# Optimization experiments

Measured on AMD Instinct MI355X. Metric: run time of the kernel, lower is better.

Reference implementation:

```python
import jax, jax.numpy as jnp
import numpy as np

FEAT = 36          # 4 + node_embedding_dim(32)
N_NODES = 24       # max_num_nodes_per_route
N_ROUTES = 48      # max_num_route
CUST_H = 128
CUST_OUT = 32
RNN_H = 128        # route_output_dim
B = 512


def _xavier(key, shape):
    fan_in, fan_out = shape[0], shape[1]
    lim = float(np.sqrt(6.0 / (fan_in + fan_out)))
    return jax.random.uniform(key, shape, jnp.float32, -lim, lim)


def setup_inputs() -> dict:
    key = jax.random.key(0)
    ks = jax.random.split(key, 24)
    inp = {
        "candidates": jax.random.normal(ks[0], (B, 2 * FEAT), jnp.float32),
        "customers": jax.random.normal(ks[1], (B, N_ROUTES, N_NODES * FEAT), jnp.float32),
        # Customer_Model MLP: 36 -> 128 (tanh) -> 32 (tanh)
        "cust_w1": _xavier(ks[2], (FEAT, CUST_H)),
        "cust_b1": jnp.zeros((CUST_H,), jnp.float32),
        "cust_w2": _xavier(ks[3], (CUST_H, CUST_OUT)),
        "cust_b2": jnp.zeros((CUST_OUT,), jnp.float32),
        # GRU layer 0 (input 32 -> hidden 128), gates order (r,z,n)
        "gru_wih0": _xavier(ks[4], (CUST_OUT, 3 * RNN_H)),
        "gru_whh0": _xavier(ks[5], (RNN_H, 3 * RNN_H)),
        "gru_bih0": jnp.zeros((3 * RNN_H,), jnp.float32),
        "gru_bhh0": jnp.zeros((3 * RNN_H,), jnp.float32),
        # GRU layer 1 (128 -> 128)
        "gru_wih1": _xavier(ks[6], (RNN_H, 3 * RNN_H)),
        "gru_whh1": _xavier(ks[7], (RNN_H, 3 * RNN_H)),
        "gru_bih1": jnp.zeros((3 * RNN_H,), jnp.float32),
        "gru_bhh1": jnp.zeros((3 * RNN_H,), jnp.float32),
        # candidate head and final MLP
        "cand_w": _xavier(ks[8], (2 * FEAT, 64)),
        "cand_b": jnp.zeros((64,), jnp.float32),
        "fc1_w": _xavier(ks[9], (RNN_H + 64, 128)),
        "fc1_b": jnp.zeros((128,), jnp.float32),
        "fc2_w": _xavier(ks[10], (128, 128)),
        "fc2_b": jnp.zeros((128,), jnp.float32),
        "fc3_w": _xavier(ks[11], (128, 1)),
        "fc3_b": jnp.zeros((1,), jnp.float32),
    }
    return inp


def _gru_layer(x_seq, wih, whh, bih, bhh):
    # x_seq: [T, N, in_dim]; returns [T, N, RNN_H]
    gi = jnp.einsum('tni,ih->tnh', x_seq, wih) + bih  # precompute input gates

    def step(h, gi_t):
        gh = h @ whh + bhh
        i_r, i_z, i_n = jnp.split(gi_t, 3, axis=-1)
        h_r, h_z, h_n = jnp.split(gh, 3, axis=-1)
        r = jax.nn.sigmoid(i_r + h_r)
        z = jax.nn.sigmoid(i_z + h_z)
        n = jnp.tanh(i_n + r * h_n)
        h_new = (1.0 - z) * n + z * h
        return h_new, h_new

    h0 = jnp.zeros((x_seq.shape[1], RNN_H), x_seq.dtype)
    _, out = jax.lax.scan(step, h0, gi)
    return out


def reference(candidates, customers, cust_w1, cust_b1, cust_w2, cust_b2,
              gru_wih0, gru_whh0, gru_bih0, gru_bhh0,
              gru_wih1, gru_whh1, gru_bih1, gru_bhh1,
              cand_w, cand_b, fc1_w, fc1_b, fc2_w, fc2_b, fc3_w, fc3_b):
    b = candidates.shape[0]
    x_c = candidates @ cand_w + cand_b                      # [B, 64]

    # all routes processed at once: fold routes into batch dim
    x = customers.reshape(b * N_ROUTES, N_NODES, FEAT)
    x = jnp.transpose(x, (1, 0, 2))                          # [T=24, B*48, 36]
    # Customer_Model MLP (tanh hidden, tanh output)
    x = jnp.tanh(jnp.tanh(x @ cust_w1 + cust_b1) @ cust_w2 + cust_b2)  # [24, B*48, 32]

    out = _gru_layer(x, gru_wih0, gru_whh0, gru_bih0, gru_bhh0)
    out = _gru_layer(out, gru_wih1, gru_whh1, gru_bih1, gru_bhh1)
    last = out[-1].reshape(b, N_ROUTES, RNN_H)               # last timestep per route
    x_r = last.mean(axis=1)                                  # mean over 48 routes
    # dropout is identity at inference

    h = jnp.concatenate([x_r, x_c], axis=1)                  # [B, 192]
    h = jnp.tanh(h @ fc1_w + fc1_b)
    h = jnp.tanh(h @ fc2_w + fc2_b)
    return h @ fc3_w + fc3_b                                 # [B, 1]
```

## Files before the change

### kernel.cpp

```cpp
#include <hip/hip_runtime.h>
#include <stdint.h>


#define NSEQ   24576
#define TSTEPS 24
#define SEQB   32

typedef __attribute__((ext_vector_type(8))) short bf16x8;
typedef __attribute__((ext_vector_type(4))) float floatx4;

#define PK_W1    0
#define PK_W2    8192
#define PK_WIH0  12288
#define PK_WHH0  24576
#define PK_WIH1  73728
#define PK_WHH1  122880
#define PK_END   172032
#define X2_EL    172032
#define HOUT_BYTE 38092800

#define MFMA(a,b,c) c = __builtin_amdgcn_mfma_f32_16x16x32_bf16(a, b, c, 0, 0, 0)

__device__ __forceinline__ uint16_t f2bf(float f) {
  uint32_t u = __float_as_uint(f);
  u += 0x7FFFu + ((u >> 16) & 1u);
  return (uint16_t)(u >> 16);
}
__device__ __forceinline__ uint32_t cvt_pk(float a, float b) {
  uint32_t r;
  asm("v_cvt_pk_bf16_f32 %0, %1, %2" : "=v"(r) : "v"(a), "v"(b));
  return r;
}
__device__ __forceinline__ float fast_sigmoid(float x) {
  float e = __builtin_amdgcn_exp2f(-1.4426950408889634f * x);
  return __builtin_amdgcn_rcpf(1.0f + e);
}
__device__ __forceinline__ float fast_tanh(float x) {
  float e = __builtin_amdgcn_exp2f(-2.8853900817779268f * x);
  return 2.0f * __builtin_amdgcn_rcpf(1.0f + e) - 1.0f;
}
__device__ __forceinline__ bf16x8 ldf(const uint16_t* p) {
  return *(const bf16x8*)p;
}

__global__ __launch_bounds__(256) void pack_weights(
    const float* __restrict__ w1, const float* __restrict__ w2,
    const float* __restrict__ wih0, const float* __restrict__ whh0,
    const float* __restrict__ wih1, const float* __restrict__ whh1,
    uint16_t* __restrict__ ws) {
  int idx = blockIdx.x * 256 + threadIdx.x;
  if (idx >= PK_END) return;
  const float* W; int N, KB, Kreal, base;
  if      (idx <  8192) { W = w1;   N = 128; KB = 2; Kreal = 36;  base = 0; }
  else if (idx < 12288) { W = w2;   N = 32;  KB = 4; Kreal = 128; base = 8192; }
  else if (idx < 24576) { W = wih0; N = 384; KB = 1; Kreal = 32;  base = 12288; }
  else if (idx < 73728) { W = whh0; N = 384; KB = 4; Kreal = 128; base = 24576; }
  else if (idx < 122880){ W = wih1; N = 384; KB = 4; Kreal = 128; base = 73728; }
  else                  { W = whh1; N = 384; KB = 4; Kreal = 128; base = 122880; }
  int li = idx - base;
  int frag = li >> 9;
  int e = li & 511;
  int lane = e >> 3, j = e & 7;
  int kb = frag % KB, nt = frag / KB;
  int k = kb * 32 + (lane >> 4) * 8 + j;
  int n = nt * 16 + (lane & 15);
  float v = (k < Kreal) ? W[k * N + n] : 0.0f;
  ws[base + li] = f2bf(v);
}

__global__ __launch_bounds__(256) void mlp_kernel(
    const float* __restrict__ customers, const float* __restrict__ b1,
    const float* __restrict__ b2, const uint16_t* __restrict__ wpk,
    uint16_t* __restrict__ x2out) {
  __shared__ uint16_t sA[128 * 136];
  const int r0 = blockIdx.x * 128;
  const int t  = r0 / NSEQ;
  const int s0 = r0 % NSEQ;
  const int tid = threadIdx.x;
  const int w = tid >> 6, l = tid & 63, q = l >> 4, c = l & 15;
  const int lo8 = l * 8;
  const int hb = 4 * q;

  floatx4 acc[2][8];
  #pragma unroll
  for (int mi = 0; mi < 2; ++mi)
    #pragma unroll
    for (int nt = 0; nt < 8; ++nt) acc[mi][nt] = (floatx4){0.f, 0.f, 0.f, 0.f};

  #pragma unroll
  for (int mi = 0; mi < 2; ++mi) {
    const int mt = 2 * w + mi;
    const int seq = s0 + mt * 16 + c;
    const float* xp = customers + (size_t)seq * 864 + t * 36;
    floatx4 u0 = *(const floatx4*)(xp + q * 8);
    floatx4 u1 = *(const floatx4*)(xp + q * 8 + 4);
    bf16x8 a0;
    { uint32_t* a0u = (uint32_t*)&a0;
      a0u[0] = cvt_pk(u0[0], u0[1]); a0u[1] = cvt_pk(u0[2], u0[3]);
      a0u[2] = cvt_pk(u1[0], u1[1]); a0u[3] = cvt_pk(u1[2], u1[3]); }
    bf16x8 a1x = (bf16x8){0,0,0,0,0,0,0,0};
    if (q == 0) {
      floatx4 u2 = *(const floatx4*)(xp + 32);
      uint32_t* a1u = (uint32_t*)&a1x;
      a1u[0] = cvt_pk(u2[0], u2[1]); a1u[1] = cvt_pk(u2[2], u2[3]);
    }
    #pragma unroll
    for (int nt = 0; nt < 8; ++nt) {
      bf16x8 bv0 = ldf(wpk + PK_W1 + (nt * 2 + 0) * 512 + lo8);
      bf16x8 bv1 = ldf(wpk + PK_W1 + (nt * 2 + 1) * 512 + lo8);
      MFMA(bv0, a0,  acc[mi][nt]);
      MFMA(bv1, a1x, acc[mi][nt]);
    }
  }
  #pragma unroll
  for (int mi = 0; mi < 2; ++mi) {
    const int mt = 2 * w + mi;
    #pragma unroll
    for (int nt = 0; nt < 8; ++nt) {
      const floatx4 bv = *(const floatx4*)(b1 + nt * 16 + hb);
      float o0 = fast_tanh(acc[mi][nt][0] + bv[0]);
      float o1 = fast_tanh(acc[mi][nt][1] + bv[1]);
      float o2 = fast_tanh(acc[mi][nt][2] + bv[2]);
      float o3 = fast_tanh(acc[mi][nt][3] + bv[3]);
      uint2 pk; pk.x = cvt_pk(o0, o1); pk.y = cvt_pk(o2, o3);
      *(uint2*)&sA[(mt * 16 + c) * 136 + nt * 16 + hb] = pk;
    }
  }
  __syncthreads();

  floatx4 acc2[2][2];
  #pragma unroll
  for (int mi = 0; mi < 2; ++mi)
    #pragma unroll
    for (int nt = 0; nt < 2; ++nt) acc2[mi][nt] = (floatx4){0.f, 0.f, 0.f, 0.f};

  #pragma unroll
  for (int kb = 0; kb < 4; ++kb) {
    bf16x8 av0 = ldf(&sA[((2 * w + 0) * 16 + c) * 136 + kb * 32 + q * 8]);
    bf16x8 av1 = ldf(&sA[((2 * w + 1) * 16 + c) * 136 + kb * 32 + q * 8]);
    #pragma unroll
    for (int nt = 0; nt < 2; ++nt) {
      bf16x8 bv = ldf(wpk + PK_W2 + (nt * 4 + kb) * 512 + lo8);
      MFMA(bv, av0, acc2[0][nt]);
      MFMA(bv, av1, acc2[1][nt]);
    }
  }
  #pragma unroll
  for (int mi = 0; mi < 2; ++mi) {
    const int mt = 2 * w + mi;
    #pragma unroll
    for (int nt = 0; nt < 2; ++nt) {
      const floatx4 bv = *(const floatx4*)(b2 + nt * 16 + hb);
      float o0 = fast_tanh(acc2[mi][nt][0] + bv[0]);
      float o1 = fast_tanh(acc2[mi][nt][1] + bv[1]);
      float o2 = fast_tanh(acc2[mi][nt][2] + bv[2]);
      float o3 = fast_tanh(acc2[mi][nt][3] + bv[3]);
      uint2 pk; pk.x = cvt_pk(o0, o1); pk.y = cvt_pk(o2, o3);
      *(uint2*)(x2out + (size_t)(r0 + mt * 16 + c) * 32 + nt * 16 + hb) = pk;
    }
  }
}

__global__ __launch_bounds__(512, 2) void gru_res(
    const uint16_t* __restrict__ wpk, const uint16_t* __restrict__ x2,
    const float* __restrict__ bih0, const float* __restrict__ bhh0,
    const float* __restrict__ bih1, const float* __restrict__ bhh1,
    float* __restrict__ hout) {
  __shared__ uint16_t h0l[2][SEQB * 136];
  __shared__ uint16_t h1l[2][SEQB * 136];
  __shared__ float bias_l[8][128];
  const int seq0 = blockIdx.x * SEQB;
  const int tid = threadIdx.x;
  const int J = tid >> 6, l = tid & 63, q = l >> 4, c = l & 15;
  const int lo8 = l * 8;

  for (int i = tid; i < 2176; i += 512) ((uint32_t*)h1l[0])[i] = 0u;
  for (int i = tid; i < 1024; i += 512) {
    int g = i >> 7, k = i & 127;
    float v;
    if      (g == 0) v = bih0[k]       + bhh0[k];
    else if (g == 1) v = bih0[128 + k] + bhh0[128 + k];
    else if (g == 2) v = bih0[256 + k];
    else if (g == 3) v = bhh0[256 + k];
    else if (g == 4) v = bih1[k]       + bhh1[k];
    else if (g == 5) v = bih1[128 + k] + bhh1[128 + k];
    else if (g == 6) v = bih1[256 + k];
    else             v = bhh1[256 + k];
    bias_l[g][k] = v;
  }

  bf16x8 wi0[3], wh0[3][4], wi1[3][4], wh1[3][4];
  #pragma unroll
  for (int g = 0; g < 3; ++g) {
    wi0[g] = ldf(wpk + PK_WIH0 + (g * 8 + J) * 512 + lo8);
    #pragma unroll
    for (int kb = 0; kb < 4; ++kb) {
      wh0[g][kb] = ldf(wpk + PK_WHH0 + ((g * 8 + J) * 4 + kb) * 512 + lo8);
      wi1[g][kb] = ldf(wpk + PK_WIH1 + ((g * 8 + J) * 4 + kb) * 512 + lo8);
      wh1[g][kb] = ldf(wpk + PK_WHH1 + ((g * 8 + J) * 4 + kb) * 512 + lo8);
    }
  }
  const int hb = J * 16 + 4 * q;

  floatx4 h0m0 = (floatx4){0.f,0.f,0.f,0.f}, h0m1 = (floatx4){0.f,0.f,0.f,0.f};
  floatx4 h1m0 = (floatx4){0.f,0.f,0.f,0.f}, h1m1 = (floatx4){0.f,0.f,0.f,0.f};

  bf16x8 ax_0 = ldf(x2 + (size_t)(seq0 + c) * 32 + q * 8);
  bf16x8 ax_1 = ldf(x2 + (size_t)(seq0 + 16 + c) * 32 + q * 8);
  __syncthreads();

  #define GRU_PRO(TI, AX, H0M)                                              \
  {                                                                         \
    floatx4 aR = *(const floatx4*)&bias_l[0][hb];                           \
    floatx4 aZ = *(const floatx4*)&bias_l[1][hb];                           \
    floatx4 aN = *(const floatx4*)&bias_l[2][hb];                           \
    floatx4 aH = *(const floatx4*)&bias_l[3][hb];                           \
    MFMA(wi0[0], AX, aR); MFMA(wi0[1], AX, aZ); MFMA(wi0[2], AX, aN);       \
    float o[4];                                                             \
    _Pragma("unroll")                                                       \
    for (int e = 0; e < 4; ++e) {                                           \
      float r  = fast_sigmoid(aR[e]);                                       \
      float zz = fast_sigmoid(aZ[e]);                                       \
      float nn = fast_tanh(aN[e] + r * aH[e]);                              \
      o[e] = nn - zz * nn;                                                  \
      H0M[e] = o[e];                                                        \
    }                                                                       \
    uint2 pk; pk.x = cvt_pk(o[0], o[1]); pk.y = cvt_pk(o[2], o[3]);         \
    *(uint2*)(h0l[0] + ((TI) * 16 + c) * 136 + hb) = pk;                    \
  }
  GRU_PRO(0, ax_0, h0m0)
  GRU_PRO(1, ax_1, h0m1)
  #undef GRU_PRO
  __syncthreads();

  ax_0 = ldf(x2 + ((size_t)NSEQ + seq0 + c) * 32 + q * 8);
  ax_1 = ldf(x2 + ((size_t)NSEQ + seq0 + 16 + c) * 32 + q * 8);

  #define GRU_TILE(TI, AX, H0M, H1M)                                        \
  {                                                                         \
    floatx4 aR1 = *(const floatx4*)&bias_l[4][hb];                          \
    floatx4 aZ1 = *(const floatx4*)&bias_l[5][hb];                          \
    floatx4 aN1 = *(const floatx4*)&bias_l[6][hb];                          \
    floatx4 aH1 = *(const floatx4*)&bias_l[7][hb];                          \
    floatx4 aR0 = *(const floatx4*)&bias_l[0][hb];                          \
    floatx4 aZ0 = *(const floatx4*)&bias_l[1][hb];                          \
    floatx4 aN0 = *(const floatx4*)&bias_l[2][hb];                          \
    floatx4 aH0 = *(const floatx4*)&bias_l[3][hb];                          \
    _Pragma("unroll")                                                       \
    for (int kb = 0; kb < 4; ++kb) {                                        \
      bf16x8 a0 = ldf(h0cur + ((TI) * 16 + c) * 136 + kb * 32 + q * 8);     \
      bf16x8 ah = ldf(h1prv + ((TI) * 16 + c) * 136 + kb * 32 + q * 8);     \
      MFMA(wi1[0][kb], a0, aR1); MFMA(wh1[0][kb], ah, aR1);                 \
      MFMA(wi1[1][kb], a0, aZ1); MFMA(wh1[1][kb], ah, aZ1);                 \
      MFMA(wi1[2][kb], a0, aN1); MFMA(wh1[2][kb], ah, aH1);                 \
      MFMA(wh0[0][kb], a0, aR0);                                            \
      MFMA(wh0[1][kb], a0, aZ0);                                            \
      MFMA(wh0[2][kb], a0, aH0);                                            \
    }                                                                       \
    MFMA(wi0[0], AX, aR0); MFMA(wi0[1], AX, aZ0); MFMA(wi0[2], AX, aN0);    \
    {                                             \
      float o[4];                                                           \
      _Pragma("unroll")                                                     \
      for (int e = 0; e < 4; ++e) {                                         \
        float r  = fast_sigmoid(aR1[e]);                                    \
        float zz = fast_sigmoid(aZ1[e]);                                    \
        float nn = fast_tanh(aN1[e] + r * aH1[e]);                          \
        o[e] = nn + zz * (H1M[e] - nn);                                     \
        H1M[e] = o[e];                                                      \
      }                                                                     \
      uint2 pk; pk.x = cvt_pk(o[0], o[1]); pk.y = cvt_pk(o[2], o[3]);       \
      *(uint2*)(h1cur + ((TI) * 16 + c) * 136 + hb) = pk;                   \
    }                                                                       \
    {                                           \
      float o[4];                                                           \
      _Pragma("unroll")                                                     \
      for (int e = 0; e < 4; ++e) {                                         \
        float r  = fast_sigmoid(aR0[e]);                                    \
        float zz = fast_sigmoid(aZ0[e]);                                    \
        float nn = fast_tanh(aN0[e] + r * aH0[e]);                          \
        o[e] = nn + zz * (H0M[e] - nn);                                     \
        H0M[e] = o[e];                                                      \
      }                                                                     \
      uint2 pk; pk.x = cvt_pk(o[0], o[1]); pk.y = cvt_pk(o[2], o[3]);       \
      *(uint2*)(h0nxt + ((TI) * 16 + c) * 136 + hb) = pk;                   \
    }                                                                       \
  }

  #pragma unroll 1
  for (int t = 0; t < TSTEPS; ++t) {
    const uint16_t* h0cur = h0l[t & 1];
    const uint16_t* h1prv = h1l[t & 1];
    uint16_t* h0nxt = h0l[(t + 1) & 1];
    uint16_t* h1cur = h1l[(t + 1) & 1];
    const int tnx = (t + 2 < TSTEPS) ? t + 2 : TSTEPS - 1;
    bf16x8 axn_0 = ldf(x2 + ((size_t)tnx * NSEQ + seq0 + c) * 32 + q * 8);
    bf16x8 axn_1 = ldf(x2 + ((size_t)tnx * NSEQ + seq0 + 16 + c) * 32 + q * 8);

    GRU_TILE(0, ax_0, h0m0, h1m0)
    __builtin_amdgcn_sched_barrier(0);
    GRU_TILE(1, ax_1, h0m1, h1m1)

    __syncthreads();
    ax_0 = axn_0; ax_1 = axn_1;
  }
  #undef GRU_TILE

  *(floatx4*)(hout + (size_t)(seq0 + c) * 128 + hb) = h1m0;
  *(floatx4*)(hout + (size_t)(seq0 + 16 + c) * 128 + hb) = h1m1;
}

__global__ __launch_bounds__(192) void final_kernel(
    const float* __restrict__ hout, const float* __restrict__ cands,
    const float* __restrict__ cw, const float* __restrict__ cb,
    const float* __restrict__ f1w, const float* __restrict__ f1b,
    const float* __restrict__ f2w, const float* __restrict__ f2b,
    const float* __restrict__ f3w, const float* __restrict__ f3b,
    float* __restrict__ out) {
  __shared__ float hc[192];
  __shared__ float v1[128];
  __shared__ float v2[128];
  __shared__ float red[128];
  const int b = blockIdx.x, tid = threadIdx.x;
  if (tid < 128) {
    float s = 0.f;
    const float* hp = hout + (size_t)(b * 48) * 128 + tid;
    #pragma unroll 4
    for (int r = 0; r < 48; ++r) s += hp[r * 128];
    hc[tid] = s * (1.0f / 48.0f);
  } else {
    int j = tid - 128;
    float s = cb[j];
    const float* cp = cands + b * 72;
    #pragma unroll 8
    for (int k = 0; k < 72; ++k) s += cp[k] * cw[k * 64 + j];
    hc[128 + j] = s;
  }
  __syncthreads();
  if (tid < 128) {
    float s = f1b[tid];
    for (int k = 0; k < 192; ++k) s += hc[k] * f1w[k * 128 + tid];
    v1[tid] = fast_tanh(s);
  }
  __syncthreads();
  if (tid < 128) {
    float s = f2b[tid];
    for (int k = 0; k < 128; ++k) s += v1[k] * f2w[k * 128 + tid];
    v2[tid] = fast_tanh(s);
  }
  __syncthreads();
  if (tid < 128) red[tid] = v2[tid] * f3w[tid];
  __syncthreads();
  if (tid < 64) {
    float s = red[tid] + red[tid + 64];
    s += __shfl_down(s, 32);
    s += __shfl_down(s, 16);
    s += __shfl_down(s, 8);
    s += __shfl_down(s, 4);
    s += __shfl_down(s, 2);
    s += __shfl_down(s, 1);
    if (tid == 0) out[b] = s + f3b[0];
  }
}

extern "C" void kernel_launch(void* const* d_in, const int* in_sizes, int n_in,
                              void* d_out, int out_size, void* d_ws, size_t ws_size,
                              hipStream_t stream) {
  const float* cand  = (const float*)d_in[0];
  const float* cust  = (const float*)d_in[1];
  const float* w1    = (const float*)d_in[2];
  const float* b1    = (const float*)d_in[3];
  const float* w2    = (const float*)d_in[4];
  const float* b2    = (const float*)d_in[5];
  const float* wih0  = (const float*)d_in[6];
  const float* whh0  = (const float*)d_in[7];
  const float* bih0  = (const float*)d_in[8];
  const float* bhh0  = (const float*)d_in[9];
  const float* wih1  = (const float*)d_in[10];
  const float* whh1  = (const float*)d_in[11];
  const float* bih1  = (const float*)d_in[12];
  const float* bhh1  = (const float*)d_in[13];
  const float* cw    = (const float*)d_in[14];
  const float* cb    = (const float*)d_in[15];
  const float* f1w   = (const float*)d_in[16];
  const float* f1b   = (const float*)d_in[17];
  const float* f2w   = (const float*)d_in[18];
  const float* f2b   = (const float*)d_in[19];
  const float* f3w   = (const float*)d_in[20];
  const float* f3b   = (const float*)d_in[21];

  uint16_t* wsp = (uint16_t*)d_ws;
  uint16_t* x2p = wsp + X2_EL;
  float* hout = (float*)((char*)d_ws + HOUT_BYTE);
  float* outp = (float*)d_out;

  pack_weights<<<(PK_END + 255) / 256, 256, 0, stream>>>(w1, w2, wih0, whh0, wih1, whh1, wsp);
  mlp_kernel<<<(NSEQ * TSTEPS) / 128, 256, 0, stream>>>(cust, b1, b2, wsp, x2p);
  gru_res<<<NSEQ / SEQB, 512, 0, stream>>>(wsp, x2p, bih0, bhh0, bih1, bhh1, hout);
  final_kernel<<<512, 192, 0, stream>>>(hout, cand, cw, cb, f1w, f1b, f2w, f2b, f3w, f3b, outp);
}
```

Baseline: 411.7 us.

## Share one reciprocal across GRU sigmoids and remap MLP blocks to timestep groups

The GRU gate math now computes the r and z sigmoids with a single reciprocal of the product (1+e_r)(1+e_z), replacing two reciprocals with one plus a few multiplies. This trims transcendental work on the serial recurrence critical path. Separately, the MLP kernel now gives each block 32 sequences across 4 timesteps (one per wave) instead of 128 sequences at one timestep, which changes the global read pattern over the customers array. The shared-reciprocal trick risks overflow or precision loss when both exponentials are large.

```diff
diff --git a/kernel.cpp b/kernel.cpp
--- a/kernel.cpp
+++ b/kernel.cpp
@@ -41,6 +41,25 @@
 }
 __device__ __forceinline__ bf16x8 ldf(const uint16_t* p) {
   return *(const bf16x8*)p;
+}
+__device__ __forceinline__ floatx4 gru_gate(floatx4 gR, floatx4 gZ,
+                                            floatx4 gN, floatx4 gH,
+                                            floatx4 hprev) {
+  floatx4 o;
+  #pragma unroll
+  for (int e = 0; e < 4; ++e) {
+    float er = __builtin_amdgcn_exp2f(-1.4426950408889634f * gR[e]);
+    float ez = __builtin_amdgcn_exp2f(-1.4426950408889634f * gZ[e]);
+    float A = 1.0f + er, B = 1.0f + ez;
+    float inv = __builtin_amdgcn_rcpf(A * B);
+    float r = B * inv;
+    float z = A * inv;
+    float m = gN[e] + r * gH[e];
+    float em = __builtin_amdgcn_exp2f(-2.8853900817779268f * m);
+    float nn = 2.0f * __builtin_amdgcn_rcpf(1.0f + em) - 1.0f;
+    o[e] = nn + z * (hprev[e] - nn);
+  }
+  return o;
 }
 
 __global__ __launch_bounds__(256) void pack_weights(
@@ -73,13 +92,15 @@
     const float* __restrict__ b2, const uint16_t* __restrict__ wpk,
     uint16_t* __restrict__ x2out) {
   __shared__ uint16_t sA[128 * 136];
-  const int r0 = blockIdx.x * 128;
-  const int t  = r0 / NSEQ;
-  const int s0 = r0 % NSEQ;
+  const int sg = blockIdx.x % 768;
+  const int tg = blockIdx.x / 768;
+  const int s0 = sg * 32;
+  const int t0 = tg * 4;
   const int tid = threadIdx.x;
   const int w = tid >> 6, l = tid & 63, q = l >> 4, c = l & 15;
   const int lo8 = l * 8;
   const int hb = 4 * q;
+  const int tw = t0 + w;
 
   floatx4 acc[2][8];
   #pragma unroll
@@ -89,9 +110,8 @@
 
   #pragma unroll
   for (int mi = 0; mi < 2; ++mi) {
-    const int mt = 2 * w + mi;
-    const int seq = s0 + mt * 16 + c;
-    const float* xp = customers + (size_t)seq * 864 + t * 36;
+    const int seq = s0 + mi * 16 + c;
+    const float* xp = customers + (size_t)seq * 864 + tw * 36;
     floatx4 u0 = *(const floatx4*)(xp + q * 8);
     floatx4 u1 = *(const floatx4*)(xp + q * 8 + 4);
     bf16x8 a0;
@@ -147,7 +167,7 @@
   }
   #pragma unroll
   for (int mi = 0; mi < 2; ++mi) {
-    const int mt = 2 * w + mi;
+    const size_t grow = (size_t)tw * NSEQ + s0 + mi * 16 + c;
     #pragma unroll
     for (int nt = 0; nt < 2; ++nt) {
       const floatx4 bv = *(const floatx4*)(b2 + nt * 16 + hb);
@@ -156,7 +176,7 @@
       float o2 = fast_tanh(acc2[mi][nt][2] + bv[2]);
       float o3 = fast_tanh(acc2[mi][nt][3] + bv[3]);
       uint2 pk; pk.x = cvt_pk(o0, o1); pk.y = cvt_pk(o2, o3);
-      *(uint2*)(x2out + (size_t)(r0 + mt * 16 + c) * 32 + nt * 16 + hb) = pk;
+      *(uint2*)(x2out + grow * 32 + nt * 16 + hb) = pk;
     }
   }
 }
@@ -204,6 +224,7 @@
 
   floatx4 h0m0 = (floatx4){0.f,0.f,0.f,0.f}, h0m1 = (floatx4){0.f,0.f,0.f,0.f};
   floatx4 h1m0 = (floatx4){0.f,0.f,0.f,0.f}, h1m1 = (floatx4){0.f,0.f,0.f,0.f};
+  const floatx4 zero4 = (floatx4){0.f,0.f,0.f,0.f};
 
   bf16x8 ax_0 = ldf(x2 + (size_t)(seq0 + c) * 32 + q * 8);
   bf16x8 ax_1 = ldf(x2 + (size_t)(seq0 + 16 + c) * 32 + q * 8);
@@ -216,16 +237,8 @@
     floatx4 aN = *(const floatx4*)&bias_l[2][hb];                           \
     floatx4 aH = *(const floatx4*)&bias_l[3][hb];                           \
     MFMA(wi0[0], AX, aR); MFMA(wi0[1], AX, aZ); MFMA(wi0[2], AX, aN);       \
-    float o[4];                                                             \
-    _Pragma("unroll")                                                       \
-    for (int e = 0; e < 4; ++e) {                                           \
-      float r  = fast_sigmoid(aR[e]);                                       \
-      float zz = fast_sigmoid(aZ[e]);                                       \
-      float nn = fast_tanh(aN[e] + r * aH[e]);                              \
-      o[e] = nn - zz * nn;                                                  \
-      H0M[e] = o[e];                                                        \
-    }                                                                       \
-    uint2 pk; pk.x = cvt_pk(o[0], o[1]); pk.y = cvt_pk(o[2], o[3]);         \
+    H0M = gru_gate(aR, aZ, aN, aH, zero4);                                  \
+    uint2 pk; pk.x = cvt_pk(H0M[0], H0M[1]); pk.y = cvt_pk(H0M[2], H0M[3]); \
     *(uint2*)(h0l[0] + ((TI) * 16 + c) * 136 + hb) = pk;                    \
   }
   GRU_PRO(0, ax_0, h0m0)
@@ -259,29 +272,13 @@
     }                                                                       \
     MFMA(wi0[0], AX, aR0); MFMA(wi0[1], AX, aZ0); MFMA(wi0[2], AX, aN0);    \
     {                                             \
-      float o[4];                                                           \
-      _Pragma("unroll")                                                     \
-      for (int e = 0; e < 4; ++e) {                                         \
-        float r  = fast_sigmoid(aR1[e]);                                    \
-        float zz = fast_sigmoid(aZ1[e]);                                    \
-        float nn = fast_tanh(aN1[e] + r * aH1[e]);                          \
-        o[e] = nn + zz * (H1M[e] - nn);                                     \
-        H1M[e] = o[e];                                                      \
-      }                                                                     \
-      uint2 pk; pk.x = cvt_pk(o[0], o[1]); pk.y = cvt_pk(o[2], o[3]);       \
+      H1M = gru_gate(aR1, aZ1, aN1, aH1, H1M);                              \
+      uint2 pk; pk.x = cvt_pk(H1M[0], H1M[1]); pk.y = cvt_pk(H1M[2], H1M[3]);\
       *(uint2*)(h1cur + ((TI) * 16 + c) * 136 + hb) = pk;                   \
     }                                                                       \
     {                                           \
-      float o[4];                                                           \
-      _Pragma("unroll")                                                     \
-      for (int e = 0; e < 4; ++e) {                                         \
-        float r  = fast_sigmoid(aR0[e]);                                    \
-        float zz = fast_sigmoid(aZ0[e]);                                    \
-        float nn = fast_tanh(aN0[e] + r * aH0[e]);                          \
-        o[e] = nn + zz * (H0M[e] - nn);                                     \
-        H0M[e] = o[e];                                                      \
-      }                                                                     \
-      uint2 pk; pk.x = cvt_pk(o[0], o[1]); pk.y = cvt_pk(o[2], o[3]);       \
+      H0M = gru_gate(aR0, aZ0, aN0, aH0, H0M);                              \
+      uint2 pk; pk.x = cvt_pk(H0M[0], H0M[1]); pk.y = cvt_pk(H0M[2], H0M[3]);\
       *(uint2*)(h0nxt + ((TI) * 16 + c) * 136 + hb) = pk;                   \
     }                                                                       \
   }
```

Measured after the change: 417.6 us. Within noise of the previous version (+1.4%).

## Regroup MLP blocks by sequence and peel final GRU step to skip dead layer-0 work

Applied to the files above, without the earlier changes.

The MLP kernel now has each block cover 32 sequences across 4 timesteps, one timestep per wave, instead of 128 consecutive rows of a single timestep. This changes the global access pattern for both the customer reads and the x2 writes. The last GRU timestep is peeled into a layer-1-only update, skipping the layer-0 computation and LDS write whose output is never used. This removes one step's worth of layer-0 MFMAs and activations, at the cost of extra code size.

```diff
diff --git a/kernel.cpp b/kernel.cpp
--- a/kernel.cpp
+++ b/kernel.cpp
@@ -73,13 +73,15 @@
     const float* __restrict__ b2, const uint16_t* __restrict__ wpk,
     uint16_t* __restrict__ x2out) {
   __shared__ uint16_t sA[128 * 136];
-  const int r0 = blockIdx.x * 128;
-  const int t  = r0 / NSEQ;
-  const int s0 = r0 % NSEQ;
+  const int sg = blockIdx.x % 768;
+  const int tg = blockIdx.x / 768;
+  const int s0 = sg * 32;
+  const int t0 = tg * 4;
   const int tid = threadIdx.x;
   const int w = tid >> 6, l = tid & 63, q = l >> 4, c = l & 15;
   const int lo8 = l * 8;
   const int hb = 4 * q;
+  const int tw = t0 + w;
 
   floatx4 acc[2][8];
   #pragma unroll
@@ -89,9 +91,8 @@
 
   #pragma unroll
   for (int mi = 0; mi < 2; ++mi) {
-    const int mt = 2 * w + mi;
-    const int seq = s0 + mt * 16 + c;
-    const float* xp = customers + (size_t)seq * 864 + t * 36;
+    const int seq = s0 + mi * 16 + c;
+    const float* xp = customers + (size_t)seq * 864 + tw * 36;
     floatx4 u0 = *(const floatx4*)(xp + q * 8);
     floatx4 u1 = *(const floatx4*)(xp + q * 8 + 4);
     bf16x8 a0;
@@ -147,7 +148,7 @@
   }
   #pragma unroll
   for (int mi = 0; mi < 2; ++mi) {
-    const int mt = 2 * w + mi;
+    const size_t grow = (size_t)tw * NSEQ + s0 + mi * 16 + c;
     #pragma unroll
     for (int nt = 0; nt < 2; ++nt) {
       const floatx4 bv = *(const floatx4*)(b2 + nt * 16 + hb);
@@ -156,7 +157,7 @@
       float o2 = fast_tanh(acc2[mi][nt][2] + bv[2]);
       float o3 = fast_tanh(acc2[mi][nt][3] + bv[3]);
       uint2 pk; pk.x = cvt_pk(o0, o1); pk.y = cvt_pk(o2, o3);
-      *(uint2*)(x2out + (size_t)(r0 + mt * 16 + c) * 32 + nt * 16 + hb) = pk;
+      *(uint2*)(x2out + grow * 32 + nt * 16 + hb) = pk;
     }
   }
 }
@@ -287,7 +288,7 @@
   }
 
   #pragma unroll 1
-  for (int t = 0; t < TSTEPS; ++t) {
+  for (int t = 0; t < TSTEPS - 1; ++t) {
     const uint16_t* h0cur = h0l[t & 1];
     const uint16_t* h1prv = h1l[t & 1];
     uint16_t* h0nxt = h0l[(t + 1) & 1];
@@ -304,6 +305,37 @@
     ax_0 = axn_0; ax_1 = axn_1;
   }
   #undef GRU_TILE
+
+  {
+    const int t = TSTEPS - 1;
+    const uint16_t* h0cur = h0l[t & 1];
+    const uint16_t* h1prv = h1l[t & 1];
+    #define GRU_LAST(TI, H1M)                                               \
+    {                                                                       \
+      floatx4 aR1 = *(const floatx4*)&bias_l[4][hb];                        \
+      floatx4 aZ1 = *(const floatx4*)&bias_l[5][hb];                        \
+      floatx4 aN1 = *(const floatx4*)&bias_l[6][hb];                        \
+      floatx4 aH1 = *(const floatx4*)&bias_l[7][hb];                        \
+      _Pragma("unroll")                                                     \
+      for (int kb = 0; kb < 4; ++kb) {                                      \
+        bf16x8 a0 = ldf(h0cur + ((TI) * 16 + c) * 136 + kb * 32 + q * 8);   \
+        bf16x8 ah = ldf(h1prv + ((TI) * 16 + c) * 136 + kb * 32 + q * 8);   \
+        MFMA(wi1[0][kb], a0, aR1); MFMA(wh1[0][kb], ah, aR1);               \
+        MFMA(wi1[1][kb], a0, aZ1); MFMA(wh1[1][kb], ah, aZ1);               \
+        MFMA(wi1[2][kb], a0, aN1); MFMA(wh1[2][kb], ah, aH1);               \
+      }                                                                     \
+      _Pragma("unroll")                                                     \
+      for (int e = 0; e < 4; ++e) {                                         \
+        float r  = fast_sigmoid(aR1[e]);                                    \
+        float zz = fast_sigmoid(aZ1[e]);                                    \
+        float nn = fast_tanh(aN1[e] + r * aH1[e]);                          \
+        H1M[e] = nn + zz * (H1M[e] - nn);                                   \
+      }                                                                     \
+    }
+    GRU_LAST(0, h1m0)
+    GRU_LAST(1, h1m1)
+    #undef GRU_LAST
+  }
 
   *(floatx4*)(hout + (size_t)(seq0 + c) * 128 + hb) = h1m0;
   *(floatx4*)(hout + (size_t)(seq0 + 16 + c) * 128 + hb) = h1m1;
```

After: 407.2 us. Within noise of the previous version (-1.1%).
